# Kernel tuning notes

Hardware: AMD Instinct MI355X
Metric: run time of the kernel (lower is better)

## Reference

```python
import jax, jax.numpy as jnp
import numpy as np


def setup_inputs() -> dict:
    key = jax.random.key(0)
    ks = jax.random.split(key, 7)
    B, S, D = 32, 1024, 1024
    R = 5
    return {
        "x": jax.random.normal(ks[0], (B, S, D), dtype=jnp.float32),
        "W": jax.random.normal(ks[1], (3 * D, D), dtype=jnp.float32) * 0.02,
        "bias": jax.random.normal(ks[2], (3 * D,), dtype=jnp.float32) * 0.02,
        "A0": jax.random.normal(ks[3], (R, D), dtype=jnp.float32) * 0.02,
        "A1": jax.random.normal(ks[4], (R, D), dtype=jnp.float32) * 0.02,
        "B0": jax.random.normal(ks[5], (D, R), dtype=jnp.float32) * 0.02,
        "B1": jax.random.normal(ks[6], (D, R), dtype=jnp.float32) * 0.02,
        "s0": jnp.ones((), dtype=jnp.float32),
        "s1": jnp.ones((), dtype=jnp.float32),
    }


def reference(x, W, bias, A0, A1, B0, B1, s0, s1):
    # weight delta: [2*out, in] = cat(s0*(B0@A0), s1*(B1@A1)), zero-padded
    # at the top to match W's rows (LoRA on K,V of a fused QKV projection).
    delta_kv = jnp.concatenate([s0 * (B0 @ A0), s1 * (B1 @ A1)], axis=0)  # [2D, D]
    pad_rows = W.shape[0] - delta_kv.shape[0]
    delta = jnp.concatenate(
        [jnp.zeros((pad_rows, W.shape[1]), dtype=W.dtype), delta_kv], axis=0
    )  # [3D, D]
    # F.linear: x @ (W + delta)^T + bias
    return jnp.einsum("bsd,od->bso", x, W + delta) + bias
```

## Files before the change

### kernel.cpp

```cpp
#include <hip/hip_runtime.h>
#include <stdint.h>

#define D_DIM 1024
#define M_DIM 32768
#define N_DIM 3072
#define K_DIM 1024
#define R_DIM 5

#define BM 128
#define BN 128
#define BK 32

typedef __bf16 bf16x8 __attribute__((ext_vector_type(8)));
typedef float  f32x4  __attribute__((ext_vector_type(4)));
typedef unsigned short ushort8 __attribute__((ext_vector_type(8)));

#define GLOBAL_AS(p) ((const __attribute__((address_space(1))) void*)(p))
#define LDS_AS(p)    ((__attribute__((address_space(3))) void*)(p))

__device__ __forceinline__ unsigned short f2bf(float f) {
    union { float f; unsigned int u; } v; v.f = f;
    unsigned int u = v.u;
    return (unsigned short)((u + 0x7fffu + ((u >> 16) & 1u)) >> 16);
}

__global__ __launch_bounds__(256) void build_weff_kernel(
    const float* __restrict__ W,
    const float* __restrict__ A0, const float* __restrict__ A1,
    const float* __restrict__ B0, const float* __restrict__ B1,
    const float* __restrict__ s0p, const float* __restrict__ s1p,
    unsigned short* __restrict__ Weff)
{
    int idx = blockIdx.x * blockDim.x + threadIdx.x;
    int o = idx >> 10;
    int c = idx & 1023;
    float w = W[idx];
    if (o >= D_DIM) {
        if (o < 2 * D_DIM) {
            const float* b = B0 + (long)(o - D_DIM) * R_DIM;
            float d = b[0] * A0[c]            + b[1] * A0[D_DIM + c]
                    + b[2] * A0[2 * D_DIM + c] + b[3] * A0[3 * D_DIM + c]
                    + b[4] * A0[4 * D_DIM + c];
            w += s0p[0] * d;
        } else {
            const float* b = B1 + (long)(o - 2 * D_DIM) * R_DIM;
            float d = b[0] * A1[c]            + b[1] * A1[D_DIM + c]
                    + b[2] * A1[2 * D_DIM + c] + b[3] * A1[3 * D_DIM + c]
                    + b[4] * A1[4 * D_DIM + c];
            w += s1p[0] * d;
        }
    }
    Weff[idx] = f2bf(w);
}

__global__ __launch_bounds__(256) void cvt_x_kernel(
    const float* __restrict__ x, unsigned short* __restrict__ xb)
{
    long idx = (long)blockIdx.x * blockDim.x + threadIdx.x;
    const f32x4* xv = (const f32x4*)x;
    f32x4 a = xv[2 * idx];
    f32x4 b = xv[2 * idx + 1];
    ushort8 r;
    r[0] = f2bf(a[0]); r[1] = f2bf(a[1]); r[2] = f2bf(a[2]); r[3] = f2bf(a[3]);
    r[4] = f2bf(b[0]); r[5] = f2bf(b[1]); r[6] = f2bf(b[2]); r[7] = f2bf(b[3]);
    *(ushort8*)(xb + 8 * idx) = r;
}

__global__ __launch_bounds__(256, 2) void gemm_kernel(
    const unsigned short* __restrict__ A,
    const unsigned short* __restrict__ Bw,
    const float* __restrict__ bias,
    float* __restrict__ C)
{
    __shared__ __align__(16) unsigned short As[BM * BK];
    __shared__ __align__(16) unsigned short Bs[BN * BK];

    const int tid  = threadIdx.x;
    const int lane = tid & 63;
    const int wave = tid >> 6;
    const int wm   = wave & 1;
    const int wn   = wave >> 1;
    const int m0   = blockIdx.y * BM;
    const int n0   = blockIdx.x * BN;

    const int srow = tid >> 2;
    const int sp   = tid & 3;
    const int sq   = sp ^ ((srow >> 1) & 3);

    const unsigned short* aSrc = A  + (long)(m0 + srow) * K_DIM + sq * 8;
    const unsigned short* bSrc = Bw + (long)(n0 + srow) * K_DIM + sq * 8;
    unsigned short* aDst = As + tid * 8;
    unsigned short* bDst = Bs + tid * 8;

    const int r16  = lane & 15;
    const int quad = lane >> 4;

    int aOff[4], bOff[4];
#pragma unroll
    for (int t = 0; t < 4; ++t) {
        int arow = wm * 64 + t * 16 + r16;
        aOff[t] = arow * BK + (quad ^ ((arow >> 1) & 3)) * 8;
        int brow = wn * 64 + t * 16 + r16;
        bOff[t] = brow * BK + (quad ^ ((brow >> 1) & 3)) * 8;
    }

    f32x4 acc[4][4] = {};

    for (int k0 = 0; k0 < K_DIM; k0 += BK) {
        __builtin_amdgcn_global_load_lds(GLOBAL_AS(aSrc + k0),              LDS_AS(aDst),        16, 0, 0);
        __builtin_amdgcn_global_load_lds(GLOBAL_AS(aSrc + 64 * K_DIM + k0), LDS_AS(aDst + 2048), 16, 0, 0);
        __builtin_amdgcn_global_load_lds(GLOBAL_AS(bSrc + k0),              LDS_AS(bDst),        16, 0, 0);
        __builtin_amdgcn_global_load_lds(GLOBAL_AS(bSrc + 64 * K_DIM + k0), LDS_AS(bDst + 2048), 16, 0, 0);
        __syncthreads();

        bf16x8 af[4], bfr[4];
#pragma unroll
        for (int t = 0; t < 4; ++t) {
            af[t]  = *(const bf16x8*)(As + aOff[t]);
            bfr[t] = *(const bf16x8*)(Bs + bOff[t]);
        }
#pragma unroll
        for (int mt = 0; mt < 4; ++mt)
#pragma unroll
            for (int nt = 0; nt < 4; ++nt)
                acc[mt][nt] = __builtin_amdgcn_mfma_f32_16x16x32_bf16(
                    af[mt], bfr[nt], acc[mt][nt], 0, 0, 0);
        __syncthreads();
    }

#pragma unroll
    for (int nt = 0; nt < 4; ++nt) {
        const int col = n0 + wn * 64 + nt * 16 + r16;
        const float bv = bias[col];
#pragma unroll
        for (int mt = 0; mt < 4; ++mt) {
            const long row = m0 + wm * 64 + mt * 16 + quad * 4;
            float* Cp = C + row * (long)N_DIM + col;
#pragma unroll
            for (int r = 0; r < 4; ++r)
                Cp[(long)r * N_DIM] = acc[mt][nt][r] + bv;
        }
    }
}

extern "C" void kernel_launch(void* const* d_in, const int* in_sizes, int n_in,
                              void* d_out, int out_size, void* d_ws, size_t ws_size,
                              hipStream_t stream) {
    const float* x    = (const float*)d_in[0];
    const float* W    = (const float*)d_in[1];
    const float* bias = (const float*)d_in[2];
    const float* A0   = (const float*)d_in[3];
    const float* A1   = (const float*)d_in[4];
    const float* B0   = (const float*)d_in[5];
    const float* B1   = (const float*)d_in[6];
    const float* s0   = (const float*)d_in[7];
    const float* s1   = (const float*)d_in[8];
    float* out = (float*)d_out;

    unsigned short* Weff = (unsigned short*)d_ws;
    unsigned short* xb   = Weff + (size_t)N_DIM * K_DIM;

    build_weff_kernel<<<(N_DIM * K_DIM) / 256, 256, 0, stream>>>(
        W, A0, A1, B0, B1, s0, s1, Weff);

    cvt_x_kernel<<<((long)M_DIM * K_DIM) / (256 * 8), 256, 0, stream>>>(x, xb);

    dim3 grid(N_DIM / BN, M_DIM / BM);
    gemm_kernel<<<grid, 256, 0, stream>>>(xb, Weff, bias, out);
}
```

Before: 713.3 us.

## Rewrite GEMM with 256x256 tiles, double-buffered LDS and phased MFMA schedule

Enlarges the GEMM tile to 256x256x64 with 512 threads and double-buffers the LDS stages. Tile k+2 is prefetched asynchronously through global_load_lds while the MFMAs run in four phases, each raised with s_setprio. Blocks are remapped across the eight XCDs for L2 locality. The aim is to hide global load latency, cut the sync stalls of the single-buffered loop, and raise reuse per LDS byte. The cost is 128KB of LDS and many accumulator registers per block, which may limit occupancy.

```diff
diff --git a/kernel.cpp b/kernel.cpp
--- a/kernel.cpp
+++ b/kernel.cpp
@@ -7,9 +7,10 @@
 #define K_DIM 1024
 #define R_DIM 5
 
-#define BM 128
-#define BN 128
-#define BK 32
+#define BM 256
+#define BN 256
+#define BK 64
+#define NKT (K_DIM / BK)
 
 typedef __bf16 bf16x8 __attribute__((ext_vector_type(8)));
 typedef float  f32x4  __attribute__((ext_vector_type(4)));
@@ -38,13 +39,13 @@
     if (o >= D_DIM) {
         if (o < 2 * D_DIM) {
             const float* b = B0 + (long)(o - D_DIM) * R_DIM;
-            float d = b[0] * A0[c]            + b[1] * A0[D_DIM + c]
+            float d = b[0] * A0[c]             + b[1] * A0[D_DIM + c]
                     + b[2] * A0[2 * D_DIM + c] + b[3] * A0[3 * D_DIM + c]
                     + b[4] * A0[4 * D_DIM + c];
             w += s0p[0] * d;
         } else {
             const float* b = B1 + (long)(o - 2 * D_DIM) * R_DIM;
-            float d = b[0] * A1[c]            + b[1] * A1[D_DIM + c]
+            float d = b[0] * A1[c]             + b[1] * A1[D_DIM + c]
                     + b[2] * A1[2 * D_DIM + c] + b[3] * A1[3 * D_DIM + c]
                     + b[4] * A1[4 * D_DIM + c];
             w += s1p[0] * d;
@@ -66,75 +67,122 @@
     *(ushort8*)(xb + 8 * idx) = r;
 }
 
-__global__ __launch_bounds__(256, 2) void gemm_kernel(
+__global__ __launch_bounds__(512, 2) void gemm_kernel(
     const unsigned short* __restrict__ A,
     const unsigned short* __restrict__ Bw,
     const float* __restrict__ bias,
     float* __restrict__ C)
 {
-    __shared__ __align__(16) unsigned short As[BM * BK];
-    __shared__ __align__(16) unsigned short Bs[BN * BK];
+    __shared__ __align__(16) unsigned short lds[2][2][BM * BK];
 
     const int tid  = threadIdx.x;
     const int lane = tid & 63;
     const int wave = tid >> 6;
-    const int wm   = wave & 1;
-    const int wn   = wave >> 1;
-    const int m0   = blockIdx.y * BM;
-    const int n0   = blockIdx.x * BN;
-
-    const int srow = tid >> 2;
-    const int sp   = tid & 3;
-    const int sq   = sp ^ ((srow >> 1) & 3);
-
-    const unsigned short* aSrc = A  + (long)(m0 + srow) * K_DIM + sq * 8;
-    const unsigned short* bSrc = Bw + (long)(n0 + srow) * K_DIM + sq * 8;
-    unsigned short* aDst = As + tid * 8;
-    unsigned short* bDst = Bs + tid * 8;
-
+    const int wm   = wave >> 2;
+    const int wnq  = wave & 3;
     const int r16  = lane & 15;
     const int quad = lane >> 4;
 
-    int aOff[4], bOff[4];
-#pragma unroll
-    for (int t = 0; t < 4; ++t) {
-        int arow = wm * 64 + t * 16 + r16;
-        aOff[t] = arow * BK + (quad ^ ((arow >> 1) & 3)) * 8;
-        int brow = wn * 64 + t * 16 + r16;
-        bOff[t] = brow * BK + (quad ^ ((brow >> 1) & 3)) * 8;
-    }
-
-    f32x4 acc[4][4] = {};
-
-    for (int k0 = 0; k0 < K_DIM; k0 += BK) {
-        __builtin_amdgcn_global_load_lds(GLOBAL_AS(aSrc + k0),              LDS_AS(aDst),        16, 0, 0);
-        __builtin_amdgcn_global_load_lds(GLOBAL_AS(aSrc + 64 * K_DIM + k0), LDS_AS(aDst + 2048), 16, 0, 0);
-        __builtin_amdgcn_global_load_lds(GLOBAL_AS(bSrc + k0),              LDS_AS(bDst),        16, 0, 0);
-        __builtin_amdgcn_global_load_lds(GLOBAL_AS(bSrc + 64 * K_DIM + k0), LDS_AS(bDst + 2048), 16, 0, 0);
-        __syncthreads();
-
-        bf16x8 af[4], bfr[4];
-#pragma unroll
-        for (int t = 0; t < 4; ++t) {
-            af[t]  = *(const bf16x8*)(As + aOff[t]);
-            bfr[t] = *(const bf16x8*)(Bs + bOff[t]);
-        }
-#pragma unroll
-        for (int mt = 0; mt < 4; ++mt)
-#pragma unroll
-            for (int nt = 0; nt < 4; ++nt)
-                acc[mt][nt] = __builtin_amdgcn_mfma_f32_16x16x32_bf16(
-                    af[mt], bfr[nt], acc[mt][nt], 0, 0, 0);
-        __syncthreads();
+    const int nwg = (M_DIM / BM) * (N_DIM / BN);
+    const int cpx = nwg / 8;
+    int bid = blockIdx.x;
+    bid = (bid % 8) * cpx + (bid / 8);
+    const int m0 = (bid / (N_DIM / BN)) * BM;
+    const int n0 = (bid % (N_DIM / BN)) * BN;
+
+    const int jrow  = tid >> 3;
+    const int chunk = (tid & 7) ^ (jrow & 7);
+    const unsigned short* aG = A  + (long)(m0 + jrow) * K_DIM + chunk * 8;
+    const unsigned short* bG = Bw + (long)(n0 + jrow) * K_DIM + chunk * 8;
+
+#define STAGE(b, t) do {                                                        \
+    const unsigned short* _as = aG + (t) * BK;                                  \
+    const unsigned short* _bs = bG + (t) * BK;                                  \
+    unsigned short* _al = &lds[b][0][0] + tid * 8;                              \
+    unsigned short* _bl = &lds[b][1][0] + tid * 8;                              \
+    _Pragma("unroll")                                                           \
+    for (int j = 0; j < 4; ++j) {                                               \
+        __builtin_amdgcn_global_load_lds(GLOBAL_AS(_as + (long)j * 64 * K_DIM), \
+                                         LDS_AS(_al + j * 4096), 16, 0, 0);     \
+        __builtin_amdgcn_global_load_lds(GLOBAL_AS(_bs + (long)j * 64 * K_DIM), \
+                                         LDS_AS(_bl + j * 4096), 16, 0, 0);     \
+    }                                                                           \
+} while (0)
+
+#define BARRIER() do { asm volatile("" ::: "memory");                 \
+                       __builtin_amdgcn_s_barrier();                  \
+                       asm volatile("" ::: "memory"); } while (0)
+#define VMCNT(n) asm volatile("s_waitcnt vmcnt(" #n ")" ::: "memory")
+
+    int sA[2];
+    sA[0] = ((0 * 4 + quad) ^ (r16 & 7)) * 8;
+    sA[1] = ((1 * 4 + quad) ^ (r16 & 7)) * 8;
+    const int arowbase = (wm * 128 + r16) * BK;
+    const int browbase = (wnq * 64 + r16) * BK;
+
+#define LDA(b, mt, kk) (*(const bf16x8*)(&lds[b][0][0] + arowbase + (mt) * 16 * BK + sA[kk]))
+#define LDB(b, nt, kk) (*(const bf16x8*)(&lds[b][1][0] + browbase + (nt) * 16 * BK + sA[kk]))
+
+    bf16x8 af[4][2];
+    bf16x8 bf[4][2];
+    f32x4  acc[8][4] = {};
+
+#define PHASE_LDA(b, msub)                                  \
+    _Pragma("unroll")                                       \
+    for (int m = 0; m < 4; ++m) {                           \
+        af[m][0] = LDA(b, (msub) * 4 + m, 0);               \
+        af[m][1] = LDA(b, (msub) * 4 + m, 1);               \
+    }
+#define PHASE_LDB(b, nsub)                                  \
+    _Pragma("unroll")                                       \
+    for (int n = 0; n < 2; ++n) {                           \
+        bf[(nsub) * 2 + n][0] = LDB(b, (nsub) * 2 + n, 0);  \
+        bf[(nsub) * 2 + n][1] = LDB(b, (nsub) * 2 + n, 1);  \
+    }
+
+#define MFMA_QUAD(ms, ns) do {                                                   \
+    __builtin_amdgcn_s_setprio(1);                                               \
+    _Pragma("unroll")                                                            \
+    for (int m = 0; m < 4; ++m)                                                  \
+    _Pragma("unroll")                                                            \
+    for (int n = 0; n < 2; ++n)                                                  \
+    _Pragma("unroll")                                                            \
+    for (int kk = 0; kk < 2; ++kk)                                               \
+        acc[(ms) * 4 + m][(ns) * 2 + n] = __builtin_amdgcn_mfma_f32_16x16x32_bf16( \
+            af[m][kk], bf[(ns) * 2 + n][kk], acc[(ms) * 4 + m][(ns) * 2 + n], 0, 0, 0); \
+    __builtin_amdgcn_s_setprio(0);                                               \
+} while (0)
+
+#define KTILE(b, tnext, dostage) do {                       \
+    PHASE_LDA(b, 0); PHASE_LDB(b, 0);                       \
+    BARRIER(); MFMA_QUAD(0, 0); BARRIER();                  \
+    PHASE_LDB(b, 1);                                        \
+    BARRIER(); MFMA_QUAD(0, 1); BARRIER();                  \
+    PHASE_LDA(b, 1);                                        \
+    BARRIER(); MFMA_QUAD(1, 0); BARRIER();                  \
+    if (dostage) { STAGE(b, tnext); VMCNT(8); }             \
+    else         { VMCNT(0); }                              \
+    BARRIER(); MFMA_QUAD(1, 1); BARRIER();                  \
+} while (0)
+
+    STAGE(0, 0);
+    STAGE(1, 1);
+    VMCNT(8);
+    BARRIER();
+
+    for (int i = 0; i < NKT / 2; ++i) {
+        const bool st = (i < NKT / 2 - 1);
+        KTILE(0, 2 * i + 2, st);
+        KTILE(1, 2 * i + 3, st);
     }
 
 #pragma unroll
     for (int nt = 0; nt < 4; ++nt) {
-        const int col = n0 + wn * 64 + nt * 16 + r16;
+        const int col = n0 + wnq * 64 + nt * 16 + r16;
         const float bv = bias[col];
 #pragma unroll
-        for (int mt = 0; mt < 4; ++mt) {
-            const long row = m0 + wm * 64 + mt * 16 + quad * 4;
+        for (int mt = 0; mt < 8; ++mt) {
+            const long row = m0 + wm * 128 + mt * 16 + quad * 4;
             float* Cp = C + row * (long)N_DIM + col;
 #pragma unroll
             for (int r = 0; r < 4; ++r)
@@ -165,6 +213,6 @@
 
     cvt_x_kernel<<<((long)M_DIM * K_DIM) / (256 * 8), 256, 0, stream>>>(x, xb);
 
-    dim3 grid(N_DIM / BN, M_DIM / BM);
-    gemm_kernel<<<grid, 256, 0, stream>>>(xb, Weff, bias, out);
-}
+    dim3 grid((M_DIM / BM) * (N_DIM / BN));
+    gemm_kernel<<<grid, 512, 0, stream>>>(xb, Weff, bias, out);
+}
```

Result: slower. 729.5 us (+2.3%).
